# Kernel optimization log

Hardware: AMD Instinct MI355X
Metric: run time of the kernel (lower is better)

The kernel has to match this reference:

```python
import math
import jax, jax.numpy as jnp
import numpy as np

N_FLOWS = 5
DIM = 64
NH = 128          # hidden multiplier -> hidden width = DIM*NH = 8192
BATCH = 4096


def _masks(out_f, in_f, dim):
    od, idd = out_f // dim, in_f // dim
    mask_d = np.zeros((out_f, in_f), np.float32)
    mask_o = np.ones((out_f, in_f), np.float32)
    for i in range(dim):
        mask_d[i * od:(i + 1) * od, i * idd:(i + 1) * idd] = 1.0
        mask_o[i * od:(i + 1) * od, i * idd:] = 0.0
    return jnp.asarray(mask_d), jnp.asarray(mask_o)

MASK_D1, MASK_O1 = _masks(DIM * NH, DIM, DIM)   # layer 1: (H, D)
MASK_D2, MASK_O2 = _masks(DIM, DIM * NH, DIM)   # layer 2: (D, H)


def masked_weight(x, W, dw, b, mask_d, mask_o, dim, grad=None):
    """MaskedWeight.forward. W:(out,in), dw:(out,1), b:(out,)."""
    out_f, in_f = W.shape
    od, idd = out_f // dim, in_f // dim
    w = jnp.exp(W) * mask_d + W * mask_o                 # (out, in)
    wsn = jnp.sum(w * w, axis=-1, keepdims=True)         # (out, 1)
    wn = jnp.exp(dw) * w / jnp.sqrt(wsn)                 # weight-normalized
    wpl = dw + W - 0.5 * jnp.log(wsn)                    # (out, in)
    # extract diagonal blocks of wpl^T: (dim, idd, od)
    blocks = wpl.reshape(dim, od, dim, idd)
    wpl_t = blocks[np.arange(dim), :, np.arange(dim), :].transpose(0, 2, 1)
    y = x @ wn.T + b                                     # (B, out)
    g = wpl_t.transpose(0, 2, 1)                         # (dim, od, idd)
    if grad is None:
        new_grad = jnp.broadcast_to(g[None], (x.shape[0],) + g.shape)
    else:
        # logsumexp over contracted block axis: out (B, dim, od, b_prev)
        new_grad = jax.nn.logsumexp(
            g[None, :, :, None, :] + jnp.swapaxes(grad, -2, -1)[:, :, None, :, :],
            axis=-1)
    return y, new_grad


def tanh_layer(x, grad):
    g = -2.0 * (x - math.log(2.0) + jax.nn.softplus(-2.0 * x))
    return jnp.tanh(x), g.reshape(grad.shape) + grad


def bnaf_flow(x, W1, d1, b1, W2, d2, b2, gate):
    h, g = masked_weight(x, W1, d1, b1, MASK_D1, MASK_O1, DIM)
    h, g = tanh_layer(h, g)
    y, g = masked_weight(h, W2, d2, b2, MASK_D2, MASK_O2, DIM, grad=g)
    grad = g[:, :, 0, 0]                                  # (B, DIM) -- squeeze
    if gate is None:                                      # res=None (last flow)
        return y, jnp.sum(grad, axis=-1)
    s = jax.nn.sigmoid(gate)                              # res='gated'
    out = s * y + (1.0 - s) * x
    ld = jnp.sum(jax.nn.softplus(grad + gate) - jax.nn.softplus(gate), axis=-1)
    return out, ld


def setup_inputs() -> dict:
    key = jax.random.key(0)
    ks = jax.random.split(key, 8)
    H = DIM * NH
    return {
        "x":  jax.random.normal(ks[0], (BATCH, DIM), jnp.float32),
        "W1": jax.random.normal(ks[1], (N_FLOWS, H, DIM), jnp.float32) * 0.1,
        "d1": jax.random.normal(ks[2], (N_FLOWS, H, 1), jnp.float32) * 0.1,
        "b1": jax.random.normal(ks[3], (N_FLOWS, H), jnp.float32) * 0.01,
        "W2": jax.random.normal(ks[4], (N_FLOWS, DIM, H), jnp.float32) * 0.1,
        "d2": jax.random.normal(ks[5], (N_FLOWS, DIM, 1), jnp.float32) * 0.1,
        "b2": jax.random.normal(ks[6], (N_FLOWS, DIM), jnp.float32) * 0.01,
        "gates": jax.random.normal(ks[7], (N_FLOWS - 1,), jnp.float32),
    }


def reference(x, W1, d1, b1, W2, d2, b2, gates):
    log_det = jnp.zeros(x.shape[0], x.dtype)
    for f in range(N_FLOWS):
        gate = gates[f] if f < N_FLOWS - 1 else None
        x, ld = bnaf_flow(x, W1[f], d1[f], b1[f], W2[f], d2[f], b2[f], gate)
        log_det = log_det + ld
        if f < N_FLOWS - 1:                               # Permutation 'flip'
            x = x[:, ::-1]
    return x, log_det
```

## Files before the change

### kernel.cpp

```cpp
#include <hip/hip_runtime.h>
#include <hip/hip_bf16.h>
#include <math.h>

#define NFLOWS 5
#define DIMF 64
#define HID 8192
#define BATCHN 4096

typedef unsigned int u32;
typedef __bf16 bf16x8 __attribute__((ext_vector_type(8)));
typedef float f32x4 __attribute__((ext_vector_type(4)));

__device__ __forceinline__ short f2bf_s(float x){
  u32 b = __float_as_uint(x);
  b += 0x7fff + ((b >> 16) & 1);
  return (short)(b >> 16);
}
__device__ __forceinline__ u32 pk_bf16(float a, float b){
#if __has_builtin(__builtin_amdgcn_cvt_pk_bf16_f32)
  typedef __bf16 bf16x2_t __attribute__((ext_vector_type(2)));
  bf16x2_t r = __builtin_amdgcn_cvt_pk_bf16_f32(a, b);
  return __builtin_bit_cast(u32, r);
#else
  u32 x = __float_as_uint(a); x += 0x7fff + ((x >> 16) & 1);
  u32 y = __float_as_uint(b); y += 0x7fff + ((y >> 16) & 1);
  return (x >> 16) | (y & 0xffff0000u);
#endif
}
__device__ __forceinline__ float softplus_f(float z){
  return fmaxf(z, 0.f) + log1pf(__expf(-fabsf(z)));
}

__global__ __launch_bounds__(256) void prep1_kernel(
    const float* __restrict__ W1, const float* __restrict__ d1,
    short* __restrict__ wn1s, float* __restrict__ g1)
{
  int w = threadIdx.x >> 6;
  int k = threadIdx.x & 63;
  int R = blockIdx.x * 4 + w;
  int rl = R & (HID - 1);
  int blk = rl >> 7;
  float Wv = W1[(size_t)R * DIMF + k];
  float wv;
  if (k == blk)      wv = __expf(Wv);
  else if (k < blk)  wv = Wv;
  else               wv = 0.f;
  float sq = wv * wv;
  #pragma unroll
  for (int m = 1; m < 64; m <<= 1) sq += __shfl_xor(sq, m, 64);
  float d1v = d1[R];
  float sc = __expf(d1v) * rsqrtf(sq);
  int f   = R >> 13;
  int i   = rl >> 7;
  int rem = rl & 127;
  int nt  = rem >> 4;
  int n16 = rem & 15;
  int ks2 = k >> 5;
  int q   = (k & 31) >> 3;
  int j   = k & 7;
  size_t dst = ((((size_t)(f * 64 + i) * 8 + nt) * 2 + ks2) << 9)
             + ((q * 16 + n16) << 3) + j;
  wn1s[dst] = f2bf_s(wv * sc);
  if (k == blk) g1[R] = d1v + Wv - 0.5f * __logf(sq);
}

__global__ __launch_bounds__(1024) void prep2_kernel(
    const float* __restrict__ W2, const float* __restrict__ d2,
    const float* __restrict__ g1,
    short* __restrict__ wn2s, float* __restrict__ expc4,
    float* __restrict__ cmax)
{
  __shared__ float red[1024];
  int f = blockIdx.x >> 6;
  int iRow = blockIdx.x & 63;
  int tid = threadIdx.x;
  const float* Wrow = W2 + ((size_t)(f * DIMF + iRow)) * HID;
  float d2v = d2[f * DIMF + iRow];
  float part = 0.f;
  #pragma unroll
  for (int kk = 0; kk < 8; ++kk) {
    int k = tid + kk * 1024;
    float Wv = Wrow[k];
    int kb = k >> 7;
    float wv = (kb == iRow) ? __expf(Wv) : ((kb < iRow) ? Wv : 0.f);
    part += wv * wv;
  }
  red[tid] = part; __syncthreads();
  for (int s = 512; s > 0; s >>= 1) {
    if (tid < s) red[tid] += red[tid + s];
    __syncthreads();
  }
  float wsn = red[0];
  __syncthreads();
  float ls = __logf(wsn);
  float sc = __expf(d2v) * rsqrtf(wsn);
  float lmax = -1e30f;
  int kheld = -1; float cvheld = 0.f;
  int mt2 = iRow >> 4, c16r = iRow & 15;
  #pragma unroll
  for (int kk = 0; kk < 8; ++kk) {
    int k = tid + kk * 1024;
    float Wv = Wrow[k];
    int kb = k >> 7;
    float wv = (kb == iRow) ? __expf(Wv) : ((kb < iRow) ? Wv : 0.f);
    int i = k >> 7, ks = (k >> 5) & 3, q = (k >> 3) & 3, j = k & 7;
    size_t dst = ((((size_t)(f * 64 + i) * 4 + ks) * 4 + mt2) << 9)
               + ((q * 16 + c16r) << 3) + j;
    wn2s[dst] = f2bf_s(wv * sc);
    if (kb == iRow) {
      float cv = g1[f * HID + k] + d2v + Wv - 0.5f * ls;
      cvheld = cv; kheld = k;
      lmax = fmaxf(lmax, cv);
    }
  }
  red[tid] = lmax; __syncthreads();
  for (int s = 512; s > 0; s >>= 1) {
    if (tid < s) red[tid] = fmaxf(red[tid], red[tid + s]);
    __syncthreads();
  }
  float M = red[0];
  if (kheld >= 0) expc4[f * HID + kheld] = 4.f * __expf(cvheld - M);
  if (tid == 0) cmax[f * DIMF + iRow] = M;
}

__global__ __launch_bounds__(1024, 4) void bnaf_main_kernel(
    const float* __restrict__ x_in,
    const float* __restrict__ b1, const float* __restrict__ b2,
    const float* __restrict__ gates,
    const short* __restrict__ wn1s,
    const short* __restrict__ wn2s,
    const float* __restrict__ expc4, const float* __restrict__ cmax,
    float* __restrict__ out)
{
  __shared__ __attribute__((aligned(16))) char smem[77184];
  float* xs  = (float*)smem;
  short* xbS = (short*)(smem + 4352);
  float* ldp = (float*)(smem + 76160);

  const int tid  = threadIdx.x;
  const int w    = tid >> 6;
  const int lane = tid & 63;
  const int c16  = lane & 15;
  const int q    = lane >> 4;
  const int r0   = blockIdx.x * 16;

  short* tsw = (short*)(smem + 6528 + w * 4352);

  {
    int row = tid >> 6, col = tid & 63;
    float v = x_in[((size_t)(r0 + row) << 6) | col];
    xs[row * 68 + col] = v;
    xbS[(col >> 3) * 136 + row * 8 + (col & 7)] = f2bf_s(v);
  }
  float ldtot = 0.f;
  __syncthreads();

  #pragma unroll 1
  for (int f = 0; f < NFLOWS; ++f) {
    const float gatev = (f < NFLOWS - 1) ? gates[f] : 0.f;
    const float spg   = (f < NFLOWS - 1) ? softplus_f(gatev) : 0.f;

    const bf16x8 xa0 = *(const bf16x8*)(xbS + q * 136 + c16 * 8);
    const bf16x8 xa1 = *(const bf16x8*)(xbS + (4 + q) * 136 + c16 * 8);

    f32x4 yacc[4];
    #pragma unroll
    for (int n = 0; n < 4; ++n) yacc[n] = f32x4{0.f, 0.f, 0.f, 0.f};
    float ldacc = 0.f;

    #pragma unroll 1
    for (int ii = 0; ii < 4; ++ii) {
      const int i = ii * 16 + w;

      const short* p1l = wn1s + (((size_t)(f * 64 + i)) << 13) + lane * 8;
      f32x4 d[8];
      #pragma unroll
      for (int nt = 0; nt < 8; ++nt) {
        bf16x8 bw0 = *(const bf16x8*)(p1l + nt * 1024);
        f32x4 z = {0.f, 0.f, 0.f, 0.f};
        d[nt] = __builtin_amdgcn_mfma_f32_16x16x32_bf16(bw0, xa0, z, 0, 0, 0);
      }
      if (i >= 32) {
        #pragma unroll
        for (int nt = 0; nt < 8; ++nt) {
          bf16x8 bw1 = *(const bf16x8*)(p1l + nt * 1024 + 512);
          d[nt] = __builtin_amdgcn_mfma_f32_16x16x32_bf16(bw1, xa1, d[nt], 0, 0, 0);
        }
      }

      const float* b1p = b1    + f * HID + i * 128 + q * 4;
      const float* ecp = expc4 + f * HID + i * 128 + q * 4;
      float sacc = 0.f;
      #pragma unroll
      for (int nt = 0; nt < 8; ++nt) {
        float4 b1q = *(const float4*)(b1p + nt * 16);
        float4 ecq = *(const float4*)(ecp + nt * 16);
        float t[4];
        #pragma unroll
        for (int r = 0; r < 4; ++r) {
          float bb = (r == 0) ? b1q.x : (r == 1) ? b1q.y : (r == 2) ? b1q.z : b1q.w;
          float ee = (r == 0) ? ecq.x : (r == 1) ? ecq.y : (r == 2) ? ecq.z : ecq.w;
          float h = d[nt][r] + bb;
          h = fminf(fmaxf(h, -30.f), 30.f);
          float u = __expf(2.f * h);
          float v = __builtin_amdgcn_rcpf(u + 1.f);
          t[r] = fmaf(-2.f, v, 1.f);
          sacc = fmaf(ee * u, v * v, sacc);
        }
        uint2 pk; pk.x = pk_bf16(t[0], t[1]); pk.y = pk_bf16(t[2], t[3]);
        *(uint2*)(tsw + c16 * 136 + nt * 16 + q * 4) = pk;
      }
      asm volatile("s_waitcnt lgkmcnt(0)" ::: "memory");

      sacc += __shfl_xor(sacc, 16, 64);
      sacc += __shfl_xor(sacc, 32, 64);
      const float Mi = cmax[f * DIMF + i];
      float grad = Mi + __logf(sacc);
      ldacc += (f < NFLOWS - 1) ? (softplus_f(grad + gatev) - spg) : grad;

      const short* p2l = wn2s + (((size_t)(f * 64 + i)) << 13) + lane * 8;
      const int mt0 = i >> 4;
      #pragma unroll
      for (int ks = 0; ks < 4; ++ks) {
        bf16x8 tb = *(const bf16x8*)(tsw + c16 * 136 + ks * 32 + q * 8);
        #pragma unroll
        for (int mt = 0; mt < 4; ++mt) {
          if (mt >= mt0) {
            bf16x8 wb = *(const bf16x8*)(p2l + (ks * 4 + mt) * 512);
            yacc[mt] = __builtin_amdgcn_mfma_f32_16x16x32_bf16(wb, tb, yacc[mt], 0, 0, 0);
          }
        }
      }
    }

    asm volatile("s_waitcnt lgkmcnt(0)" ::: "memory");
    float* ypw = (float*)(smem + 6528 + w * 4352);
    #pragma unroll
    for (int mt = 0; mt < 4; ++mt)
      #pragma unroll
      for (int r = 0; r < 4; ++r)
        ypw[(mt * 4 + r) * 64 + lane] = yacc[mt][r];
    if (q == 0) ldp[w * 16 + c16] = ldacc;
    __syncthreads();

    float sgate = 0.f;
    if (f < NFLOWS - 1) sgate = __builtin_amdgcn_rcpf(1.f + __expf(-gatev));
    int row = tid >> 6, col = tid & 63;
    int idx = (((col >> 4) * 4 + (col & 3)) * 64) + (((col >> 2) & 3) * 16) + row;
    float v = b2[f * DIMF + col];
    #pragma unroll
    for (int ww = 0; ww < 16; ++ww)
      v += ((const float*)(smem + 6528 + ww * 4352))[idx];
    float nx = 0.f; int nrow = 0, ncol = 0;
    if (f < NFLOWS - 1) {
      float xv = xs[row * 68 + col];
      nx = fmaf(sgate, v - xv, xv);
      nrow = row; ncol = 63 - col;
    } else {
      out[((size_t)(r0 + row) << 6) | col] = v;
    }
    if (tid < 16) {
      float a = 0.f;
      #pragma unroll
      for (int ww = 0; ww < 16; ++ww) a += ldp[ww * 16 + tid];
      ldtot += a;
    }
    __syncthreads();
    if (f < NFLOWS - 1) {
      xs[nrow * 68 + ncol] = nx;
      xbS[(ncol >> 3) * 136 + nrow * 8 + (ncol & 7)] = f2bf_s(nx);
      __syncthreads();
    }
  }

  if (tid < 16) out[(size_t)BATCHN * DIMF + r0 + tid] = ldtot;
}

extern "C" void kernel_launch(void* const* d_in, const int* in_sizes, int n_in,
                              void* d_out, int out_size, void* d_ws, size_t ws_size,
                              hipStream_t stream)
{
  const float* x     = (const float*)d_in[0];
  const float* W1    = (const float*)d_in[1];
  const float* d1    = (const float*)d_in[2];
  const float* b1    = (const float*)d_in[3];
  const float* W2    = (const float*)d_in[4];
  const float* d2    = (const float*)d_in[5];
  const float* b2    = (const float*)d_in[6];
  const float* gates = (const float*)d_in[7];
  float* out = (float*)d_out;

  char* ws = (char*)d_ws;
  short* wn1s  = (short*)ws;
  short* wn2s  = (short*)(ws + 5242880);
  float* expc4 = (float*)(ws + 10485760);
  float* cmaxp = (float*)(ws + 10649600);
  float* g1    = (float*)(ws + 10650880);

  hipLaunchKernelGGL(prep1_kernel, dim3(10240), dim3(256), 0, stream, W1, d1, wn1s, g1);
  hipLaunchKernelGGL(prep2_kernel, dim3(320), dim3(1024), 0, stream, W2, d2, g1, wn2s, expc4, cmaxp);
  hipLaunchKernelGGL(bnaf_main_kernel, dim3(256), dim3(1024), 0, stream,
                     x, b1, b2, gates, wn1s, wn2s, expc4, cmaxp, out);
}
```

Before: 284.5 us.

## Software-pipeline second-layer MFMA, fold bias into accumulator, rewrite prep2 per-wave

```diff
diff --git a/kernel.cpp b/kernel.cpp
--- a/kernel.cpp
+++ b/kernel.cpp
@@ -64,63 +64,86 @@
   if (k == blk) g1[R] = d1v + Wv - 0.5f * __logf(sq);
 }
 
-__global__ __launch_bounds__(1024) void prep2_kernel(
+__global__ __launch_bounds__(256) void prep2_kernel(
     const float* __restrict__ W2, const float* __restrict__ d2,
     const float* __restrict__ g1,
     short* __restrict__ wn2s, float* __restrict__ expc4,
     float* __restrict__ cmax)
 {
-  __shared__ float red[1024];
-  int f = blockIdx.x >> 6;
-  int iRow = blockIdx.x & 63;
-  int tid = threadIdx.x;
+  int wid  = blockIdx.x * 4 + (threadIdx.x >> 6);
+  int lane = threadIdx.x & 63;
+  int f = wid >> 6, iRow = wid & 63;
   const float* Wrow = W2 + ((size_t)(f * DIMF + iRow)) * HID;
   float d2v = d2[f * DIMF + iRow];
-  float part = 0.f;
+  int mt2 = iRow >> 4, c16r = iRow & 15;
+
+  float p0 = 0.f, p1 = 0.f;
+  #pragma unroll 4
+  for (int it = 0; it < 16; ++it) {
+    int k0 = it * 512 + lane * 8;
+    int kb = k0 >> 7;
+    float4 a = *(const float4*)(Wrow + k0);
+    float4 b = *(const float4*)(Wrow + k0 + 4);
+    float wv[8] = {a.x, a.y, a.z, a.w, b.x, b.y, b.z, b.w};
+    if (kb == iRow) {
+      #pragma unroll
+      for (int e = 0; e < 8; ++e) wv[e] = __expf(wv[e]);
+    } else if (kb > iRow) {
+      #pragma unroll
+      for (int e = 0; e < 8; ++e) wv[e] = 0.f;
+    }
+    p0 += wv[0]*wv[0] + wv[1]*wv[1] + wv[2]*wv[2] + wv[3]*wv[3];
+    p1 += wv[4]*wv[4] + wv[5]*wv[5] + wv[6]*wv[6] + wv[7]*wv[7];
+  }
+  float part = p0 + p1;
   #pragma unroll
-  for (int kk = 0; kk < 8; ++kk) {
-    int k = tid + kk * 1024;
-    float Wv = Wrow[k];
-    int kb = k >> 7;
-    float wv = (kb == iRow) ? __expf(Wv) : ((kb < iRow) ? Wv : 0.f);
-    part += wv * wv;
-  }
-  red[tid] = part; __syncthreads();
-  for (int s = 512; s > 0; s >>= 1) {
-    if (tid < s) red[tid] += red[tid + s];
-    __syncthreads();
-  }
-  float wsn = red[0];
-  __syncthreads();
-  float ls = __logf(wsn);
-  float sc = __expf(d2v) * rsqrtf(wsn);
-  float lmax = -1e30f;
-  int kheld = -1; float cvheld = 0.f;
-  int mt2 = iRow >> 4, c16r = iRow & 15;
+  for (int m = 1; m < 64; m <<= 1) part += __shfl_xor(part, m, 64);
+  float ls = __logf(part);
+  float sc = __expf(d2v) * rsqrtf(part);
+
+  float cvr[8]; int k0d = -1; float lm = -1e30f;
+  #pragma unroll 4
+  for (int it = 0; it < 16; ++it) {
+    int k0 = it * 512 + lane * 8;
+    int kb = k0 >> 7;
+    float4 a = *(const float4*)(Wrow + k0);
+    float4 b = *(const float4*)(Wrow + k0 + 4);
+    float wv[8] = {a.x, a.y, a.z, a.w, b.x, b.y, b.z, b.w};
+    if (kb == iRow) {
+      float4 ga = *(const float4*)(g1 + f * HID + k0);
+      float4 gb = *(const float4*)(g1 + f * HID + k0 + 4);
+      float gg[8] = {ga.x, ga.y, ga.z, ga.w, gb.x, gb.y, gb.z, gb.w};
+      #pragma unroll
+      for (int e = 0; e < 8; ++e) {
+        cvr[e] = gg[e] + d2v + wv[e] - 0.5f * ls;
+        lm = fmaxf(lm, cvr[e]);
+        wv[e] = __expf(wv[e]);
+      }
+      k0d = k0;
+    } else if (kb > iRow) {
+      #pragma unroll
+      for (int e = 0; e < 8; ++e) wv[e] = 0.f;
+    }
+    int i = k0 >> 7, ks = (k0 >> 5) & 3, qq = (k0 >> 3) & 3;
+    size_t dst = ((((size_t)(f * 64 + i) * 4 + ks) * 4 + mt2) << 9)
+               + ((qq * 16 + c16r) << 3);
+    uint4 pk4;
+    pk4.x = pk_bf16(wv[0]*sc, wv[1]*sc); pk4.y = pk_bf16(wv[2]*sc, wv[3]*sc);
+    pk4.z = pk_bf16(wv[4]*sc, wv[5]*sc); pk4.w = pk_bf16(wv[6]*sc, wv[7]*sc);
+    *(uint4*)(wn2s + dst) = pk4;
+  }
   #pragma unroll
-  for (int kk = 0; kk < 8; ++kk) {
-    int k = tid + kk * 1024;
-    float Wv = Wrow[k];
-    int kb = k >> 7;
-    float wv = (kb == iRow) ? __expf(Wv) : ((kb < iRow) ? Wv : 0.f);
-    int i = k >> 7, ks = (k >> 5) & 3, q = (k >> 3) & 3, j = k & 7;
-    size_t dst = ((((size_t)(f * 64 + i) * 4 + ks) * 4 + mt2) << 9)
-               + ((q * 16 + c16r) << 3) + j;
-    wn2s[dst] = f2bf_s(wv * sc);
-    if (kb == iRow) {
-      float cv = g1[f * HID + k] + d2v + Wv - 0.5f * ls;
-      cvheld = cv; kheld = k;
-      lmax = fmaxf(lmax, cv);
-    }
-  }
-  red[tid] = lmax; __syncthreads();
-  for (int s = 512; s > 0; s >>= 1) {
-    if (tid < s) red[tid] = fmaxf(red[tid], red[tid + s]);
-    __syncthreads();
-  }
-  float M = red[0];
-  if (kheld >= 0) expc4[f * HID + kheld] = 4.f * __expf(cvheld - M);
-  if (tid == 0) cmax[f * DIMF + iRow] = M;
+  for (int m = 1; m < 64; m <<= 1) lm = fmaxf(lm, __shfl_xor(lm, m, 64));
+  if (k0d >= 0) {
+    float4 ea, eb;
+    ea.x = 4.f*__expf(cvr[0]-lm); ea.y = 4.f*__expf(cvr[1]-lm);
+    ea.z = 4.f*__expf(cvr[2]-lm); ea.w = 4.f*__expf(cvr[3]-lm);
+    eb.x = 4.f*__expf(cvr[4]-lm); eb.y = 4.f*__expf(cvr[5]-lm);
+    eb.z = 4.f*__expf(cvr[6]-lm); eb.w = 4.f*__expf(cvr[7]-lm);
+    *(float4*)(expc4 + f * HID + k0d)     = ea;
+    *(float4*)(expc4 + f * HID + k0d + 4) = eb;
+  }
+  if (lane == 0) cmax[f * DIMF + iRow] = lm;
 }
 
 __global__ __launch_bounds__(1024, 4) void bnaf_main_kernel(
@@ -132,10 +155,10 @@
     const float* __restrict__ expc4, const float* __restrict__ cmax,
     float* __restrict__ out)
 {
-  __shared__ __attribute__((aligned(16))) char smem[77184];
+  __shared__ __attribute__((aligned(16))) char smem[146816];
   float* xs  = (float*)smem;
   short* xbS = (short*)(smem + 4352);
-  float* ldp = (float*)(smem + 76160);
+  float* ldp = (float*)(smem + 145792);
 
   const int tid  = threadIdx.x;
   const int w    = tid >> 6;
@@ -144,7 +167,8 @@
   const int q    = lane >> 4;
   const int r0   = blockIdx.x * 16;
 
-  short* tsw = (short*)(smem + 6528 + w * 4352);
+  short* tbuf0 = (short*)(smem + 6528 + w * 8704);
+  short* tbuf1 = (short*)(smem + 6528 + w * 8704 + 4352);
 
   {
     int row = tid >> 6, col = tid & 63;
@@ -171,13 +195,16 @@
     #pragma unroll 1
     for (int ii = 0; ii < 4; ++ii) {
       const int i = ii * 16 + w;
+      short* tb = (ii & 1) ? tbuf1 : tbuf0;
 
       const short* p1l = wn1s + (((size_t)(f * 64 + i)) << 13) + lane * 8;
+      const float* b1p = b1 + f * HID + i * 128 + q * 4;
       f32x4 d[8];
       #pragma unroll
       for (int nt = 0; nt < 8; ++nt) {
+        float4 b1q = *(const float4*)(b1p + nt * 16);
+        f32x4 z = {b1q.x, b1q.y, b1q.z, b1q.w};
         bf16x8 bw0 = *(const bf16x8*)(p1l + nt * 1024);
-        f32x4 z = {0.f, 0.f, 0.f, 0.f};
         d[nt] = __builtin_amdgcn_mfma_f32_16x16x32_bf16(bw0, xa0, z, 0, 0, 0);
       }
       if (i >= 32) {
@@ -188,69 +215,91 @@
         }
       }
 
-      const float* b1p = b1    + f * HID + i * 128 + q * 4;
+      if (ii > 0) {
+        const int ip = i - 16;
+        short* tp = ((ii - 1) & 1) ? tbuf1 : tbuf0;
+        asm volatile("s_waitcnt lgkmcnt(0)" ::: "memory");
+        const short* p2l = wn2s + (((size_t)(f * 64 + ip)) << 13) + lane * 8;
+        const int mt0 = ip >> 4;
+        #pragma unroll
+        for (int ks = 0; ks < 4; ++ks) {
+          bf16x8 tfrag = *(const bf16x8*)(tp + c16 * 136 + ks * 32 + q * 8);
+          #pragma unroll
+          for (int mt = 0; mt < 4; ++mt) {
+            if (mt >= mt0) {
+              bf16x8 wb = *(const bf16x8*)(p2l + (ks * 4 + mt) * 512);
+              yacc[mt] = __builtin_amdgcn_mfma_f32_16x16x32_bf16(wb, tfrag, yacc[mt], 0, 0, 0);
+            }
+          }
+        }
+      }
+
       const float* ecp = expc4 + f * HID + i * 128 + q * 4;
-      float sacc = 0.f;
+      const float Mi = cmax[f * DIMF + i];
+      float s0 = 0.f, s1 = 0.f, s2 = 0.f, s3 = 0.f;
       #pragma unroll
       for (int nt = 0; nt < 8; ++nt) {
-        float4 b1q = *(const float4*)(b1p + nt * 16);
         float4 ecq = *(const float4*)(ecp + nt * 16);
         float t[4];
         #pragma unroll
         for (int r = 0; r < 4; ++r) {
-          float bb = (r == 0) ? b1q.x : (r == 1) ? b1q.y : (r == 2) ? b1q.z : b1q.w;
           float ee = (r == 0) ? ecq.x : (r == 1) ? ecq.y : (r == 2) ? ecq.z : ecq.w;
-          float h = d[nt][r] + bb;
-          h = fminf(fmaxf(h, -30.f), 30.f);
-          float u = __expf(2.f * h);
-          float v = __builtin_amdgcn_rcpf(u + 1.f);
-          t[r] = fmaf(-2.f, v, 1.f);
-          sacc = fmaf(ee * u, v * v, sacc);
+          float h  = d[nt][r];
+          float up = __expf(-2.f * fabsf(h));
+          float vp = __builtin_amdgcn_rcpf(1.f + up);
+          float ta = fmaf(-2.f * up, vp, 1.f);
+          t[r] = copysignf(ta, h);
+          float c1 = ee * up, c2 = vp * vp;
+          if (r == 0) s0 = fmaf(c1, c2, s0);
+          else if (r == 1) s1 = fmaf(c1, c2, s1);
+          else if (r == 2) s2 = fmaf(c1, c2, s2);
+          else s3 = fmaf(c1, c2, s3);
         }
         uint2 pk; pk.x = pk_bf16(t[0], t[1]); pk.y = pk_bf16(t[2], t[3]);
-        *(uint2*)(tsw + c16 * 136 + nt * 16 + q * 4) = pk;
-      }
-      asm volatile("s_waitcnt lgkmcnt(0)" ::: "memory");
-
+        *(uint2*)(tb + c16 * 136 + nt * 16 + q * 4) = pk;
+      }
+      float sacc = (s0 + s1) + (s2 + s3);
       sacc += __shfl_xor(sacc, 16, 64);
       sacc += __shfl_xor(sacc, 32, 64);
-      const float Mi = cmax[f * DIMF + i];
       float grad = Mi + __logf(sacc);
       ldacc += (f < NFLOWS - 1) ? (softplus_f(grad + gatev) - spg) : grad;
-
-      const short* p2l = wn2s + (((size_t)(f * 64 + i)) << 13) + lane * 8;
-      const int mt0 = i >> 4;
+    }
+
+    {
+      const int ip = 48 + w;
+      asm volatile("s_waitcnt lgkmcnt(0)" ::: "memory");
+      const short* p2l = wn2s + (((size_t)(f * 64 + ip)) << 13) + lane * 8;
+      const int mt0 = ip >> 4;
       #pragma unroll
       for (int ks = 0; ks < 4; ++ks) {
-        bf16x8 tb = *(const bf16x8*)(tsw + c16 * 136 + ks * 32 + q * 8);
+        bf16x8 tfrag = *(const bf16x8*)(tbuf1 + c16 * 136 + ks * 32 + q * 8);
         #pragma unroll
         for (int mt = 0; mt < 4; ++mt) {
           if (mt >= mt0) {
             bf16x8 wb = *(const bf16x8*)(p2l + (ks * 4 + mt) * 512);
-            yacc[mt] = __builtin_amdgcn_mfma_f32_16x16x32_bf16(wb, tb, yacc[mt], 0, 0, 0);
+            yacc[mt] = __builtin_amdgcn_mfma_f32_16x16x32_bf16(wb, tfrag, yacc[mt], 0, 0, 0);
           }
         }
       }
     }
 
-    asm volatile("s_waitcnt lgkmcnt(0)" ::: "memory");
-    float* ypw = (float*)(smem + 6528 + w * 4352);
+    float* ypw = (float*)(smem + 6528 + w * 8704);
     #pragma unroll
     for (int mt = 0; mt < 4; ++mt)
       #pragma unroll
       for (int r = 0; r < 4; ++r)
-        ypw[(mt * 4 + r) * 64 + lane] = yacc[mt][r];
+        ypw[(mt * 4 + r) * 65 + lane] = yacc[mt][r];
     if (q == 0) ldp[w * 16 + c16] = ldacc;
     __syncthreads();
 
     float sgate = 0.f;
     if (f < NFLOWS - 1) sgate = __builtin_amdgcn_rcpf(1.f + __expf(-gatev));
     int row = tid >> 6, col = tid & 63;
-    int idx = (((col >> 4) * 4 + (col & 3)) * 64) + (((col >> 2) & 3) * 16) + row;
+    int idx = ((col >> 4) * 4 + (col & 3)) * 65 + (((col >> 2) & 3) * 16 + row);
     float v = b2[f * DIMF + col];
     #pragma unroll
     for (int ww = 0; ww < 16; ++ww)
-      v += ((const float*)(smem + 6528 + ww * 4352))[idx];
+      v += ((const float*)(smem + 6528 + ww * 8704))[idx];
     float nx = 0.f; int nrow = 0, ncol = 0;
     if (f < NFLOWS - 1) {
       float xv = xs[row * 68 + col];
@@ -298,7 +347,7 @@
   float* g1    = (float*)(ws + 10650880);
 
   hipLaunchKernelGGL(prep1_kernel, dim3(10240), dim3(256), 0, stream, W1, d1, wn1s, g1);
-  hipLaunchKernelGGL(prep2_kernel, dim3(320), dim3(1024), 0, stream, W2, d2, g1, wn2s, expc4, cmaxp);
+  hipLaunchKernelGGL(prep2_kernel, dim3(80), dim3(256), 0, stream, W2, d2, g1, wn2s, expc4, cmaxp);
   hipLaunchKernelGGL(bnaf_main_kernel, dim3(256), dim3(1024), 0, stream,
                      x, b1, b2, gates, wn1s, wn2s, expc4, cmaxp, out);
 }
```

Measured after the change: 398.7 us. +40.1%, slower.
